# Kernel optimization log

Hardware: AMD Instinct MI355X
Metric: run time of the kernel (lower is better)

## Reference

```python
import jax, jax.numpy as jnp
import numpy as np

N, M, DIST, HEADS, D, C, DFFN = 16384, 16, 2, 8, 256, 64, 512
DH = D // HEADS
GRID = 128
BLOCK = 2048  # mirrors torch batch_size loop in find_neighboring_voxels_optimized
EPS = 1e-5


def _neighbors(coords_f, src, m, dist):
    """Blockwise Manhattan-distance topk neighbor gather.
    coords_f: (N,3) float voxel coords; src: (N,D) features.
    Returns (N, m, D) neighbor features, zero-filled where fewer than m in range."""
    n = coords_f.shape[0]
    qblocks = coords_f.reshape(-1, BLOCK, 3)

    def one_block(cb):
        # (BLOCK, N) Manhattan distances
        d = jnp.abs(cb[:, None, :] - coords_f[None, :, :]).sum(-1)
        d = jnp.where(d <= dist, d, jnp.inf)
        vals, idx = jax.lax.top_k(-d, m)          # nearest m (self first: dist 0)
        valid = (vals > -jnp.inf)[..., None]
        return jnp.where(valid, src[idx], jnp.zeros((), src.dtype))

    return jax.lax.map(one_block, qblocks).reshape(n, m, src.shape[-1])


def _layernorm(x, g, b):
    mu = x.mean(-1, keepdims=True)
    var = ((x - mu) ** 2).mean(-1, keepdims=True)
    return (x - mu) * jax.lax.rsqrt(var + EPS) * g + b


def setup_inputs() -> dict:
    key = jax.random.key(0)
    ks = jax.random.split(key, 32)
    p = lambda i, shape, s: jax.random.normal(ks[i], shape, dtype=jnp.float32) * s
    z = lambda shape: jnp.zeros(shape, dtype=jnp.float32)
    o = lambda shape: jnp.ones(shape, dtype=jnp.float32)
    return {
        "coords": jax.random.randint(ks[0], (N, 3), 0, GRID, dtype=jnp.int32),
        "features": jax.random.normal(ks[1], (N, C), dtype=jnp.float32),
        "pe_w1": p(2, (3, D // 2), 0.5), "pe_b1": z((D // 2,)),
        "pe_w2": p(3, (D // 2, D), 0.08), "pe_b2": z((D,)),
        "proj_w": p(4, (C, D), 0.12), "proj_b": z((D,)),
        "wq": p(5, (D, D), 0.06), "bq": z((D,)),
        "wk": p(6, (D, D), 0.06), "bk": z((D,)),
        "wv": p(7, (D, D), 0.06), "bv": z((D,)),
        "wo": p(8, (D, D), 0.06), "bo": z((D,)),
        "ffn_w1": p(9, (D, DFFN), 0.06), "ffn_b1": z((DFFN,)),
        "ffn_w2": p(10, (DFFN, D), 0.04), "ffn_b2": z((D,)),
        "ln_g": o((D,)), "ln_b": z((D,)),
        "fus_w1": p(11, (D, C), 0.06), "fus_b1": z((C,)),
        "fus_w2": p(12, (2 * C, C), 0.09), "fus_b2": z((C,)),
        "bn_g": o((C,)), "bn_b": z((C,)),
    }


def reference(coords, features, pe_w1, pe_b1, pe_w2, pe_b2, proj_w, proj_b,
              wq, bq, wk, bk, wv, bv, wo, bo,
              ffn_w1, ffn_b1, ffn_w2, ffn_b2, ln_g, ln_b,
              fus_w1, fus_b1, fus_w2, fus_b2, bn_g, bn_b):
    coords_f = coords.astype(jnp.float32)
    # dynamic learnable positional encoding on normalized coords
    xn = coords_f / (GRID - 1)
    pe = jax.nn.relu(xn @ pe_w1 + pe_b1) @ pe_w2 + pe_b2
    src = features @ proj_w + proj_b + pe                       # (N, D)

    nf = _neighbors(coords_f, src, M, DIST)                     # (N, M, D)
    query = nf[:, 0, :]                                         # (N, D) self-feature

    # multihead attention: query len 1, key len M, batch N
    q = (query @ wq + bq).reshape(N, HEADS, DH)
    k = (nf @ wk + bk).reshape(N, M, HEADS, DH)
    v = (nf @ wv + bv).reshape(N, M, HEADS, DH)
    scores = jnp.einsum('nhd,nmhd->nhm', q, k) / jnp.sqrt(jnp.float32(DH))
    attn = jax.nn.softmax(scores, axis=-1)
    ao = jnp.einsum('nhm,nmhd->nhd', attn, v).reshape(N, D) @ wo + bo  # (N, D)

    # FFN with residual + LayerNorm (dropout=0 / eval)
    h = jax.nn.relu(ao @ ffn_w1 + ffn_b1) @ ffn_w2 + ffn_b2
    y = _layernorm(ao + h, ln_g, ln_b)                          # (N, D)

    # EnhancedFusion: project, concat, linear, BatchNorm1d (batch stats), ReLU
    t = y @ fus_w1 + fus_b1                                     # (N, C)
    f = jnp.concatenate([features, t], axis=1) @ fus_w2 + fus_b2
    mu = f.mean(0)
    var = ((f - mu) ** 2).mean(0)
    f = (f - mu) * jax.lax.rsqrt(var + EPS) * bn_g + bn_b
    return jax.nn.relu(f)                                       # (N, C)
```

## Files before the change

### kernel.cpp

```cpp
#include <hip/hip_runtime.h>
#include <stdint.h>

typedef unsigned short u16;
typedef unsigned int   u32;
typedef __attribute__((ext_vector_type(8))) short short8;
typedef __attribute__((ext_vector_type(4))) float f32x4;

static constexpr int kN = 16384;
static constexpr float kEPS = 1e-5f;

__device__ __forceinline__ u16 f2bf(float x) {
  u32 u = __float_as_uint(x);
  u32 r = (u + 0x7fffu + ((u >> 16) & 1u)) >> 16;
  return (u16)r;
}
__device__ __forceinline__ float bf2f(u16 x) {
  return __uint_as_float(((u32)x) << 16);
}
__device__ __forceinline__ void ldbf8(const u16* p, float* o) {
  uint4 v = *(const uint4*)p;
  o[0] = __uint_as_float(v.x << 16);  o[1] = __uint_as_float(v.x & 0xffff0000u);
  o[2] = __uint_as_float(v.y << 16);  o[3] = __uint_as_float(v.y & 0xffff0000u);
  o[4] = __uint_as_float(v.z << 16);  o[5] = __uint_as_float(v.z & 0xffff0000u);
  o[6] = __uint_as_float(v.w << 16);  o[7] = __uint_as_float(v.w & 0xffff0000u);
}
__device__ __forceinline__ void gll16(const u16* g, u16* l) {
  __builtin_amdgcn_global_load_lds(
      (const __attribute__((address_space(1))) void*)g,
      (__attribute__((address_space(3))) void*)l, 16, 0, 0);
}

struct WSet {
  const float* s[8]; u16* d[8];
  int K[8]; int N[8]; int dstride[8]; int coff[8];
};

__global__ __launch_bounds__(256) void k_setup(WSet ws,
                                               u32* __restrict__ zero_area,
                                               const float* __restrict__ proj_b,
                                               const float* __restrict__ pe_b2,
                                               float* __restrict__ pbc,
                                               const float* __restrict__ uw1,
                                               const float* __restrict__ ub1,
                                               const float* __restrict__ uw2,
                                               const float* __restrict__ ub2,
                                               u16* __restrict__ W2f,
                                               float* __restrict__ bbf,
                                               const int* __restrict__ coords,
                                               const float* __restrict__ feats,
                                               const float* __restrict__ pw1,
                                               const float* __restrict__ pb1,
                                               u16* __restrict__ A1,
                                               u16* __restrict__ A2) {
  int w = blockIdx.y;
  if (w == 8) {
    int idx = blockIdx.x * 256 + threadIdx.x;
    if (idx < 33088) zero_area[idx] = 0u;
    return;
  }
  if (w == 9) {
    int bx = blockIdx.x;
    if (bx == 0) {
      pbc[threadIdx.x] = proj_b[threadIdx.x] + pe_b2[threadIdx.x];
    } else if (bx < 65) {
      int n = bx - 1;
      int k = threadIdx.x;
      float s = 0.f;
      for (int j = 0; j < 64; j++) s += uw1[k * 64 + j] * uw2[(64 + j) * 64 + n];
      W2f[n * 320 + k] = f2bf(s);
      if (k < 64) W2f[n * 320 + 256 + k] = f2bf(uw2[k * 64 + n]);
      if (k == 0) {
        float b = ub2[n];
        for (int j = 0; j < 64; j++) b += ub1[j] * uw2[(64 + j) * 64 + n];
        bbf[n] = b;
      }
    }
    return;
  }
  if (w == 10) {
    int r0 = blockIdx.x * 32;
#pragma unroll
    for (int s = 0; s < 3; s++) {
      int j = threadIdx.x + s * 256;
      int row = j / 24, seg = j % 24;
      int n = r0 + row;
      u16 o[8];
      if (seg < 8) {
        const float* fp = feats + (size_t)n * 64 + seg * 8;
        float4 a = *(const float4*)fp;
        float4 b = *(const float4*)(fp + 4);
        o[0] = f2bf(a.x); o[1] = f2bf(a.y); o[2] = f2bf(a.z); o[3] = f2bf(a.w);
        o[4] = f2bf(b.x); o[5] = f2bf(b.y); o[6] = f2bf(b.z); o[7] = f2bf(b.w);
        *(uint4*)(A2 + (size_t)n * 320 + 256 + seg * 8) = *(uint4*)o;
      } else {
        int jj0 = (seg - 8) * 8;
        float x0 = (float)coords[n * 3 + 0] * (1.f / 127.f);
        float x1 = (float)coords[n * 3 + 1] * (1.f / 127.f);
        float x2 = (float)coords[n * 3 + 2] * (1.f / 127.f);
#pragma unroll
        for (int u = 0; u < 8; u++) {
          int jj = jj0 + u;
          float hv = pb1[jj] + x0 * pw1[jj] + x1 * pw1[128 + jj] + x2 * pw1[256 + jj];
          o[u] = f2bf(fmaxf(hv, 0.f));
        }
      }
      *(uint4*)(A1 + (size_t)n * 192 + seg * 8) = *(uint4*)o;
    }
    return;
  }
  const float* S = ws.s[w]; u16* D = ws.d[w];
  int K = ws.K[w], N = ws.N[w], ds = ws.dstride[w], co = ws.coff[w];
  int ntx = N >> 5, tiles = ntx * (K >> 5);
  int t = blockIdx.x;
  if (t >= tiles) return;
  int n0 = (t % ntx) * 32, k0 = (t / ntx) * 32;
  __shared__ float st[32][33];
  int tr = threadIdx.x >> 3, tc4 = (threadIdx.x & 7) * 4;
  float4 v = *(const float4*)(S + (size_t)(k0 + tr) * N + n0 + tc4);
  st[tc4 + 0][tr] = v.x; st[tc4 + 1][tr] = v.y;
  st[tc4 + 2][tr] = v.z; st[tc4 + 3][tr] = v.w;
  __syncthreads();
  u16 o4[4];
  o4[0] = f2bf(st[tr][tc4 + 0]); o4[1] = f2bf(st[tr][tc4 + 1]);
  o4[2] = f2bf(st[tr][tc4 + 2]); o4[3] = f2bf(st[tr][tc4 + 3]);
  *(uint2*)(D + (size_t)(n0 + tr) * ds + co + k0 + tc4) = *(uint2*)o4;
}


__global__ __launch_bounds__(256) void k_hist(const int* __restrict__ coords,
                                              u32* __restrict__ cnt) {
  int n = blockIdx.x * 256 + threadIdx.x;
  int c = coords[n * 3] * 128 + coords[n * 3 + 1];
  atomicAdd(&cnt[c], 1u);
}

__global__ __launch_bounds__(256) void k_scan(const u32* __restrict__ cnt,
                                              u32* __restrict__ startb) {
  __shared__ u32 tots[256];
  int t = threadIdx.x;
  int base = t * 64;
  u32 s = 0;
  for (int i = 0; i < 64; i++) s += cnt[base + i];
  tots[t] = s;
  __syncthreads();
  if (t == 0) {
    u32 run = 0;
    for (int i = 0; i < 256; i++) { u32 v = tots[i]; tots[i] = run; run += v; }
  }
  __syncthreads();
  u32 run = tots[t];
  for (int i = 0; i < 64; i++) { startb[base + i] = run; run += cnt[base + i]; }
}

__global__ __launch_bounds__(256) void k_scatter(const int* __restrict__ coords,
                                                 const u32* __restrict__ startb,
                                                 u32* __restrict__ cursor,
                                                 u32* __restrict__ pts) {
  int n = blockIdx.x * 256 + threadIdx.x;
  int x = coords[n * 3], y = coords[n * 3 + 1], z = coords[n * 3 + 2];
  int c = x * 128 + y;
  u32 slot = atomicAdd(&cursor[c], 1u);
  pts[startb[c] + slot] = ((u32)z << 14) | (u32)n;
}

__global__ __launch_bounds__(256) void k_select(const int* __restrict__ coords,
                                                const u32* __restrict__ startb,
                                                const u32* __restrict__ cnt,
                                                const u32* __restrict__ pts,
                                                int* __restrict__ idxo) {
  int n = blockIdx.x * 256 + threadIdx.x;
  int x = coords[n * 3], y = coords[n * 3 + 1], z = coords[n * 3 + 2];
  u32 best[16];
#pragma unroll
  for (int j = 0; j < 16; j++) best[j] = 0xFFFFFFFFu;
  const int dxs[13] = {0, -1, 1, 0, 0, -2, 2, 0, 0, -1, -1, 1, 1};
  const int dys[13] = {0, 0, 0, -1, 1, 0, 0, -2, 2, -1, 1, -1, 1};
  const int dbs[13] = {0, 1, 1, 1, 1, 2, 2, 2, 2, 2, 2, 2, 2};
#pragma unroll
  for (int t = 0; t < 13; t++) {
    int xx = x + dxs[t], yy = y + dys[t];
    if (xx < 0 || xx > 127 || yy < 0 || yy > 127) continue;
    int c = xx * 128 + yy;
    u32 s0 = startb[c], e0 = s0 + cnt[c];
    for (u32 i = s0; i < e0; ++i) {
      u32 p = pts[i];
      int zq = (int)(p >> 14);
      int id = (int)(p & 16383u);
      int az = z - zq; az = az < 0 ? -az : az;
      int dd = dbs[t] + az;
      u32 key = (dd <= 2) ? (((u32)dd << 14) | (u32)id) : 0xFFFFFFFFu;
#pragma unroll
      for (int j = 0; j < 16; j++) {
        u32 lo = min(best[j], key);
        u32 hi = max(best[j], key);
        best[j] = lo; key = hi;
      }
    }
  }
#pragma unroll
  for (int j = 0; j < 16; j++)
    idxo[n * 16 + j] = (best[j] == 0xFFFFFFFFu) ? -1 : (int)(best[j] & 16383u);
}

template <int ACT, int OUTBF, int ADD>
__global__ __launch_bounds__(256) void k_mfma_gemm(
    const u16* __restrict__ A, const u16* __restrict__ WT,
    const float* __restrict__ bias,
    void* __restrict__ Cout,
    const u16* __restrict__ Addp,
    int M, int K, int N) {
  __shared__ __align__(16) u16 As[2][64 * 32];
  __shared__ __align__(16) u16 Bs[2][64 * 32];
  const int tid = threadIdx.x;
  const int wave = tid >> 6, lane = tid & 63;
  const int bm = blockIdx.y * 64, bn = blockIdx.x * 64;
  const int wr = (wave >> 1) * 32, wc = (wave & 1) * 32;
  const int g = wave * 64 + lane;
  const int grow = g >> 2, gko = (g & 3) * 8;
  const int fr = lane & 15, fk = (lane >> 4) * 8, rq = (lane >> 4) * 4;

  f32x4 acc[2][2];
#pragma unroll
  for (int i = 0; i < 2; i++)
#pragma unroll
    for (int j = 0; j < 2; j++)
#pragma unroll
      for (int r = 0; r < 4; r++) acc[i][j][r] = 0.f;

  for (int k0 = 0; k0 < K; k0 += 64) {
#pragma unroll
    for (int h = 0; h < 2; h++) {
      gll16(A + (size_t)(bm + grow) * K + k0 + h * 32 + gko, As[h] + g * 8);
      gll16(WT + (size_t)(bn + grow) * K + k0 + h * 32 + gko, Bs[h] + g * 8);
    }
    __syncthreads();
#pragma unroll
    for (int h = 0; h < 2; h++) {
      short8 af[2], bg[2];
#pragma unroll
      for (int i = 0; i < 2; i++)
        af[i] = *(const short8*)&As[h][(wr + i * 16 + fr) * 32 + fk];
#pragma unroll
      for (int j = 0; j < 2; j++)
        bg[j] = *(const short8*)&Bs[h][(wc + j * 16 + fr) * 32 + fk];
#pragma unroll
      for (int i = 0; i < 2; i++)
#pragma unroll
        for (int j = 0; j < 2; j++)
          acc[i][j] = __builtin_amdgcn_mfma_f32_16x16x32_bf16(af[i], bg[j], acc[i][j], 0, 0, 0);
    }
    __syncthreads();
  }

#pragma unroll
  for (int j = 0; j < 2; j++) {
    int cc = bn + wc + j * 16 + fr;
    float bval = bias ? bias[cc] : 0.f;
#pragma unroll
    for (int i = 0; i < 2; i++) {
      int rbase = bm + wr + i * 16 + rq;
#pragma unroll
      for (int r = 0; r < 4; r++) {
        float v = acc[i][j][r] + bval;
        size_t o = (size_t)(rbase + r) * N + cc;
        if (ADD) v += bf2f(Addp[o]);
        if (ACT) v = fmaxf(v, 0.f);
        if (OUTBF) ((u16*)Cout)[o] = f2bf(v);
        else       ((float*)Cout)[o] = v;
      }
    }
  }
}

__global__ __launch_bounds__(256) void k_attn(const u16* __restrict__ QKV,
                                              const u32* __restrict__ pts,
                                              const int* __restrict__ idx,
                                              const float* __restrict__ bq,
                                              const float* __restrict__ bk,
                                              const float* __restrict__ bv,
                                              u16* __restrict__ outp) {
  int gid = blockIdx.x * 256 + threadIdx.x;
  int n = (int)(pts[gid >> 3] & 16383u), h = gid & 7;
  const int* ip = idx + n * 16;
  const int hb = h * 32;
  float q[32];
  {
    int i0 = ip[0];
    const u16* qp = QKV + (size_t)i0 * 768 + hb;
#pragma unroll
    for (int j = 0; j < 32; j += 8) ldbf8(qp + j, &q[j]);
#pragma unroll
    for (int j = 0; j < 32; j++) q[j] += bq[hb + j];
  }
  float qbk = 0.f;
#pragma unroll
  for (int j = 0; j < 32; j++) qbk += q[j] * bk[hb + j];
  float s[16]; int ii[16];
#pragma unroll
  for (int m = 0; m < 16; m++) {
    int i = ip[m]; ii[m] = i;
    float d = qbk;
    if (i >= 0) {
      const u16* kp = QKV + (size_t)i * 768 + 256 + hb;
      float kv[32];
#pragma unroll
      for (int j = 0; j < 32; j += 8) ldbf8(kp + j, &kv[j]);
#pragma unroll
      for (int j = 0; j < 32; j++) d += q[j] * kv[j];
    }
    s[m] = d * 0.17677669529663689f;
  }
  float mx = s[0];
#pragma unroll
  for (int m = 1; m < 16; m++) mx = fmaxf(mx, s[m]);
  float sum = 0.f;
#pragma unroll
  for (int m = 0; m < 16; m++) { s[m] = __expf(s[m] - mx); sum += s[m]; }
  float inv = 1.f / sum;
  float o[32];
#pragma unroll
  for (int j = 0; j < 32; j++) o[j] = 0.f;
#pragma unroll
  for (int m = 0; m < 16; m++) {
    if (ii[m] >= 0) {
      const u16* vp = QKV + (size_t)ii[m] * 768 + 512 + hb;
      float vv[32];
#pragma unroll
      for (int j = 0; j < 32; j += 8) ldbf8(vp + j, &vv[j]);
#pragma unroll
      for (int j = 0; j < 32; j++) o[j] += s[m] * vv[j];
    }
  }
  u16* op = outp + (size_t)n * 256 + hb;
#pragma unroll
  for (int j = 0; j < 32; j += 8) {
    u16 tmp[8];
#pragma unroll
    for (int jj = 0; jj < 8; jj++) tmp[jj] = f2bf(o[j + jj] * inv + bv[hb + j + jj]);
    *(uint4*)(op + j) = *(uint4*)tmp;
  }
}

__global__ __launch_bounds__(256) void k_ln(const u16* __restrict__ xx,
                                            const float* __restrict__ g,
                                            const float* __restrict__ b,
                                            u16* __restrict__ A2) {
  int row = blockIdx.x * 4 + (threadIdx.x >> 6);
  int lane = threadIdx.x & 63;
  uint2 raw = *(const uint2*)(xx + (size_t)row * 256 + lane * 4);
  float x0 = __uint_as_float(raw.x << 16), x1 = __uint_as_float(raw.x & 0xffff0000u);
  float x2 = __uint_as_float(raw.y << 16), x3 = __uint_as_float(raw.y & 0xffff0000u);
  float sm = x0 + x1 + x2 + x3;
#pragma unroll
  for (int off = 1; off < 64; off <<= 1) sm += __shfl_xor(sm, off);
  float mu = sm * (1.f / 256.f);
  float d0 = x0 - mu, d1 = x1 - mu, d2 = x2 - mu, d3 = x3 - mu;
  float sq = d0 * d0 + d1 * d1 + d2 * d2 + d3 * d3;
#pragma unroll
  for (int off = 1; off < 64; off <<= 1) sq += __shfl_xor(sq, off);
  float rstd = rsqrtf(sq * (1.f / 256.f) + kEPS);
  float4 gv = *(const float4*)(g + lane * 4);
  float4 bv4 = *(const float4*)(b + lane * 4);
  u16 o[4];
  o[0] = f2bf(d0 * rstd * gv.x + bv4.x); o[1] = f2bf(d1 * rstd * gv.y + bv4.y);
  o[2] = f2bf(d2 * rstd * gv.z + bv4.z); o[3] = f2bf(d3 * rstd * gv.w + bv4.w);
  *(uint2*)(A2 + (size_t)row * 320 + lane * 4) = *(uint2*)o;
}

__global__ __launch_bounds__(256) void k_fgemm(const u16* __restrict__ A2,
                                               const u16* __restrict__ W2f,
                                               const float* __restrict__ bbf,
                                               float* __restrict__ fB,
                                               float* __restrict__ pS,
                                               float* __restrict__ pQ) {
  __shared__ __align__(16) u16 As[2][2048];
  __shared__ __align__(16) u16 Bs[2][2048];
  __shared__ float colS[64][2], colQ[64][2];
  const int tid = threadIdx.x;
  const int wave = tid >> 6, lane = tid & 63;
  const int bm = blockIdx.x * 64;
  const int wr = (wave >> 1) * 32, wc = (wave & 1) * 32;
  const int fr = lane & 15, fk = (lane >> 4) * 8, rq = (lane >> 4) * 4;
  const int g = wave * 64 + lane;
  const int grow = g >> 2, gko = (g & 3) * 8;

  f32x4 acc[2][2];
#pragma unroll
  for (int i = 0; i < 2; i++)
#pragma unroll
    for (int j = 0; j < 2; j++)
#pragma unroll
      for (int r = 0; r < 4; r++) acc[i][j][r] = 0.f;
  for (int k0 = 0; k0 < 320; k0 += 64) {
#pragma unroll
    for (int h = 0; h < 2; h++) {
      gll16(A2 + (size_t)(bm + grow) * 320 + k0 + h * 32 + gko, As[h] + g * 8);
      gll16(W2f + (size_t)grow * 320 + k0 + h * 32 + gko, Bs[h] + g * 8);
    }
    __syncthreads();
#pragma unroll
    for (int h = 0; h < 2; h++) {
      short8 af[2], bg[2];
#pragma unroll
      for (int i = 0; i < 2; i++)
        af[i] = *(const short8*)&As[h][(wr + i * 16 + fr) * 32 + fk];
#pragma unroll
      for (int j = 0; j < 2; j++)
        bg[j] = *(const short8*)&Bs[h][(wc + j * 16 + fr) * 32 + fk];
#pragma unroll
      for (int i = 0; i < 2; i++)
#pragma unroll
        for (int j = 0; j < 2; j++)
          acc[i][j] = __builtin_amdgcn_mfma_f32_16x16x32_bf16(af[i], bg[j], acc[i][j], 0, 0, 0);
    }
    __syncthreads();
  }
  float cS[2] = {0.f, 0.f}, cQ[2] = {0.f, 0.f};
#pragma unroll
  for (int j = 0; j < 2; j++) {
    int col = wc + j * 16 + fr;
    float bv = bbf[col];
#pragma unroll
    for (int i = 0; i < 2; i++) {
      int rbase = bm + wr + i * 16 + rq;
#pragma unroll
      for (int r = 0; r < 4; r++) {
        float v = acc[i][j][r] + bv;
        fB[(size_t)(rbase + r) * 64 + col] = v;
        cS[j] += v; cQ[j] += v * v;
      }
    }
  }
#pragma unroll
  for (int off = 16; off < 64; off <<= 1) {
#pragma unroll
    for (int j = 0; j < 2; j++) {
      cS[j] += __shfl_xor(cS[j], off);
      cQ[j] += __shfl_xor(cQ[j], off);
    }
  }
  if ((lane >> 4) == 0) {
#pragma unroll
    for (int j = 0; j < 2; j++) {
      colS[wc + j * 16 + fr][wave >> 1] = cS[j];
      colQ[wc + j * 16 + fr][wave >> 1] = cQ[j];
    }
  }
  __syncthreads();
  if (tid < 64) {
    atomicAdd(&pS[tid], colS[tid][0] + colS[tid][1]);
    atomicAdd(&pQ[tid], colQ[tid][0] + colQ[tid][1]);
  }
}

__global__ __launch_bounds__(64) void k_bnfin(const float* __restrict__ pS,
                                              const float* __restrict__ pQ,
                                              const float* __restrict__ g,
                                              const float* __restrict__ b,
                                              float* __restrict__ coef,
                                              float* __restrict__ shift) {
  int c = threadIdx.x;
  float S = pS[c], Q = pQ[c];
  float m = S * (1.f / 16384.f);
  float var = Q * (1.f / 16384.f) - m * m;
  float cf = rsqrtf(var + kEPS) * g[c];
  coef[c] = cf;
  shift[c] = b[c] - m * cf;
}

__global__ __launch_bounds__(256) void k_bnapply(const float* __restrict__ f,
                                                 const float* __restrict__ coef,
                                                 const float* __restrict__ shift,
                                                 float* __restrict__ out) {
  int gid = blockIdx.x * 256 + threadIdx.x;
  int e = gid * 4, col = e & 63;
  float4 v = *(const float4*)(f + e);
  float4 cf = *(const float4*)(coef + col);
  float4 sh = *(const float4*)(shift + col);
  float4 o;
  o.x = fmaxf(v.x * cf.x + sh.x, 0.f);
  o.y = fmaxf(v.y * cf.y + sh.y, 0.f);
  o.z = fmaxf(v.z * cf.z + sh.z, 0.f);
  o.w = fmaxf(v.w * cf.w + sh.w, 0.f);
  *(float4*)(out + e) = o;
}

extern "C" void kernel_launch(void* const* d_in, const int* in_sizes, int n_in,
                              void* d_out, int out_size, void* d_ws, size_t ws_size,
                              hipStream_t stream) {
  (void)in_sizes; (void)n_in; (void)out_size; (void)ws_size;
  const int*   coords = (const int*)d_in[0];
  const float* feats  = (const float*)d_in[1];
  const float* pe_w1  = (const float*)d_in[2];
  const float* pe_b1  = (const float*)d_in[3];
  const float* pe_w2  = (const float*)d_in[4];
  const float* pe_b2  = (const float*)d_in[5];
  const float* proj_w = (const float*)d_in[6];
  const float* proj_b = (const float*)d_in[7];
  const float* wq  = (const float*)d_in[8];
  const float* bq  = (const float*)d_in[9];
  const float* wk  = (const float*)d_in[10];
  const float* bk  = (const float*)d_in[11];
  const float* wv  = (const float*)d_in[12];
  const float* bv  = (const float*)d_in[13];
  const float* wo  = (const float*)d_in[14];
  const float* bo  = (const float*)d_in[15];
  const float* fw1 = (const float*)d_in[16];
  const float* fb1 = (const float*)d_in[17];
  const float* fw2 = (const float*)d_in[18];
  const float* fb2 = (const float*)d_in[19];
  const float* lng = (const float*)d_in[20];
  const float* lnb = (const float*)d_in[21];
  const float* uw1 = (const float*)d_in[22];
  const float* ub1 = (const float*)d_in[23];
  const float* uw2 = (const float*)d_in[24];
  const float* ub2 = (const float*)d_in[25];
  const float* bng = (const float*)d_in[26];
  const float* bnb = (const float*)d_in[27];
  float* out = (float*)d_out;

  char* Wc = (char*)d_ws;
  const size_t MB = 1u << 20;
  u16*   A1    = (u16*)(Wc + 0 * MB);
  u16*   srcb  = (u16*)(Wc + 6 * MB);
  u16*   QKVb  = (u16*)(Wc + 14 * MB);
  u16*   aoInB = (u16*)(Wc + 38 * MB);
  u16*   aoB   = (u16*)(Wc + 46 * MB);
  u16*   h1B   = (u16*)(Wc + 54 * MB);
  u16*   xBb   = (u16*)(Wc + 70 * MB);
  u16*   A2    = (u16*)(Wc + 78 * MB);
  float* fB    = (float*)(Wc + 0 * MB);

  u16* qkvT  = (u16*)(Wc + 88 * MB);
  u16* woT   = qkvT + 196608;
  u16* fw1T  = woT + 65536;
  u16* fw2T  = fw1T + 131072;
  u16* W1T   = fw2T + 131072;
  u16* W2f   = W1T + 49152;
  float* pbc = (float*)(W2f + 20480);
  float* bbf = pbc + 256;

  u32* Z      = (u32*)(Wc + 90 * MB);
  u32* cnt    = Z;
  u32* cursor = Z + 16384;
  float* pS   = (float*)(Z + 32768);
  float* pQ   = (float*)(Z + 32832);
  float* coefb = (float*)(Z + 32912);
  float* shb   = coefb + 64;
  u32* startb = Z + 33280;
  u32* pts    = Z + 49664;
  int* idxb   = (int*)(Z + 66048);

  WSet ws;
  ws.s[0] = wq;     ws.d[0] = qkvT;          ws.K[0] = 256; ws.N[0] = 256; ws.dstride[0] = 256; ws.coff[0] = 0;
  ws.s[1] = wk;     ws.d[1] = qkvT + 65536;  ws.K[1] = 256; ws.N[1] = 256; ws.dstride[1] = 256; ws.coff[1] = 0;
  ws.s[2] = wv;     ws.d[2] = qkvT + 131072; ws.K[2] = 256; ws.N[2] = 256; ws.dstride[2] = 256; ws.coff[2] = 0;
  ws.s[3] = wo;     ws.d[3] = woT;           ws.K[3] = 256; ws.N[3] = 256; ws.dstride[3] = 256; ws.coff[3] = 0;
  ws.s[4] = fw1;    ws.d[4] = fw1T;          ws.K[4] = 256; ws.N[4] = 512; ws.dstride[4] = 256; ws.coff[4] = 0;
  ws.s[5] = fw2;    ws.d[5] = fw2T;          ws.K[5] = 512; ws.N[5] = 256; ws.dstride[5] = 512; ws.coff[5] = 0;
  ws.s[6] = proj_w; ws.d[6] = W1T;           ws.K[6] = 64;  ws.N[6] = 256; ws.dstride[6] = 192; ws.coff[6] = 0;
  ws.s[7] = pe_w2;  ws.d[7] = W1T;           ws.K[7] = 128; ws.N[7] = 256; ws.dstride[7] = 192; ws.coff[7] = 64;

  k_setup<<<dim3(512, 11), 256, 0, stream>>>(ws, Z, proj_b, pe_b2, pbc,
                                             uw1, ub1, uw2, ub2, W2f, bbf,
                                             coords, feats, pe_w1, pe_b1, A1, A2);
  k_hist<<<64, 256, 0, stream>>>(coords, cnt);
  k_scan<<<1, 256, 0, stream>>>(cnt, startb);
  k_scatter<<<64, 256, 0, stream>>>(coords, startb, cursor, pts);
  k_select<<<64, 256, 0, stream>>>(coords, startb, cnt, pts, idxb);
  k_mfma_gemm<0, 1, 0><<<dim3(4, 256), 256, 0, stream>>>(A1, W1T, pbc, srcb, nullptr, kN, 192, 256);
  k_mfma_gemm<0, 1, 0><<<dim3(12, 256), 256, 0, stream>>>(srcb, qkvT, nullptr, QKVb, nullptr, kN, 256, 768);
  k_attn<<<512, 256, 0, stream>>>(QKVb, pts, idxb, bq, bk, bv, aoInB);
  k_mfma_gemm<0, 1, 0><<<dim3(4, 256), 256, 0, stream>>>(aoInB, woT, bo, aoB, nullptr, kN, 256, 256);
  k_mfma_gemm<1, 1, 0><<<dim3(8, 256), 256, 0, stream>>>(aoB, fw1T, fb1, h1B, nullptr, kN, 256, 512);
  k_mfma_gemm<0, 1, 1><<<dim3(4, 256), 256, 0, stream>>>(h1B, fw2T, fb2, xBb, aoB, kN, 512, 256);
  k_ln<<<4096, 256, 0, stream>>>(xBb, lng, lnb, A2);
  k_fgemm<<<256, 256, 0, stream>>>(A2, W2f, bbf, fB, pS, pQ);
  k_bnfin<<<1, 64, 0, stream>>>(pS, pQ, bng, bnb, coefb, shb);
  k_bnapply<<<1024, 256, 0, stream>>>(fB, coefb, shb, out);
}
```

Measured before the change: 248.1 us.

## Fold input projection into QKV weights and enlarge MFMA GEMM tiles

```diff
diff --git a/kernel.cpp b/kernel.cpp
--- a/kernel.cpp
+++ b/kernel.cpp
@@ -31,15 +31,14 @@
 }
 
 struct WSet {
-  const float* s[8]; u16* d[8];
-  int K[8]; int N[8]; int dstride[8]; int coff[8];
+  const float* s[6]; u16* d[6];
+  int K[6]; int N[6]; int dstride[6]; int coff[6];
 };
 
 __global__ __launch_bounds__(256) void k_setup(WSet ws,
                                                u32* __restrict__ zero_area,
                                                const float* __restrict__ proj_b,
                                                const float* __restrict__ pe_b2,
-                                               float* __restrict__ pbc,
                                                const float* __restrict__ uw1,
                                                const float* __restrict__ ub1,
                                                const float* __restrict__ uw2,
@@ -51,33 +50,36 @@
                                                const float* __restrict__ pw1,
                                                const float* __restrict__ pb1,
                                                u16* __restrict__ A1,
-                                               u16* __restrict__ A2) {
+                                               u16* __restrict__ A2,
+                                               const float* __restrict__ wq,
+                                               const float* __restrict__ wk,
+                                               const float* __restrict__ wv,
+                                               const float* __restrict__ proj_w_f,
+                                               const float* __restrict__ pe_w2_f,
+                                               u16* __restrict__ W1K,
+                                               float* __restrict__ bcomb) {
   int w = blockIdx.y;
-  if (w == 8) {
+  if (w == 6) {
     int idx = blockIdx.x * 256 + threadIdx.x;
     if (idx < 33088) zero_area[idx] = 0u;
     return;
   }
-  if (w == 9) {
-    int bx = blockIdx.x;
-    if (bx == 0) {
-      pbc[threadIdx.x] = proj_b[threadIdx.x] + pe_b2[threadIdx.x];
-    } else if (bx < 65) {
-      int n = bx - 1;
-      int k = threadIdx.x;
-      float s = 0.f;
-      for (int j = 0; j < 64; j++) s += uw1[k * 64 + j] * uw2[(64 + j) * 64 + n];
-      W2f[n * 320 + k] = f2bf(s);
-      if (k < 64) W2f[n * 320 + 256 + k] = f2bf(uw2[k * 64 + n]);
-      if (k == 0) {
-        float b = ub2[n];
-        for (int j = 0; j < 64; j++) b += ub1[j] * uw2[(64 + j) * 64 + n];
-        bbf[n] = b;
-      }
+  if (w == 7) {
+    int n = blockIdx.x;
+    if (n >= 64) return;
+    int k = threadIdx.x;
+    float s = 0.f;
+    for (int j = 0; j < 64; j++) s += uw1[k * 64 + j] * uw2[(64 + j) * 64 + n];
+    W2f[n * 320 + k] = f2bf(s);
+    if (k < 64) W2f[n * 320 + 256 + k] = f2bf(uw2[k * 64 + n]);
+    if (k == 0) {
+      float b = ub2[n];
+      for (int j = 0; j < 64; j++) b += ub1[j] * uw2[(64 + j) * 64 + n];
+      bbf[n] = b;
     }
     return;
   }
-  if (w == 10) {
+  if (w == 8) {
     int r0 = blockIdx.x * 32;
 #pragma unroll
     for (int s = 0; s < 3; s++) {
@@ -108,6 +110,26 @@
     }
     return;
   }
+  if (w == 9) {
+    int bx = blockIdx.x;
+    if (bx < 3) {
+      const float* wsel = (bx == 0) ? wq : (bx == 1) ? wk : wv;
+      int c = threadIdx.x;
+      float s = 0.f;
+      for (int d = 0; d < 256; d++) s += (proj_b[d] + pe_b2[d]) * wsel[d * 256 + c];
+      bcomb[bx * 256 + c] = s;
+    } else if (bx < 27) {
+      int i0 = (bx - 3) * 2048 + threadIdx.x * 8;
+      const float* src = (i0 < 16384) ? (proj_w_f + i0) : (pe_w2_f + (i0 - 16384));
+      float4 a = *(const float4*)src;
+      float4 b = *(const float4*)(src + 4);
+      u16 o[8];
+      o[0] = f2bf(a.x); o[1] = f2bf(a.y); o[2] = f2bf(a.z); o[3] = f2bf(a.w);
+      o[4] = f2bf(b.x); o[5] = f2bf(b.y); o[6] = f2bf(b.z); o[7] = f2bf(b.w);
+      *(uint4*)(W1K + i0) = *(uint4*)o;
+    }
+    return;
+  }
   const float* S = ws.s[w]; u16* D = ws.d[w];
   int K = ws.K[w], N = ws.N[w], ds = ws.dstride[w], co = ws.coff[w];
   int ntx = N >> 5, tiles = ntx * (K >> 5);
@@ -202,62 +224,72 @@
     idxo[n * 16 + j] = (best[j] == 0xFFFFFFFFu) ? -1 : (int)(best[j] & 16383u);
 }
 
-template <int ACT, int OUTBF, int ADD>
-__global__ __launch_bounds__(256) void k_mfma_gemm(
+template <int BM, int BN, int ACT, int OUTBF, int ADD>
+__global__ __launch_bounds__(256) void k_mgemm(
     const u16* __restrict__ A, const u16* __restrict__ WT,
     const float* __restrict__ bias,
     void* __restrict__ Cout,
     const u16* __restrict__ Addp,
     int M, int K, int N) {
-  __shared__ __align__(16) u16 As[2][64 * 32];
-  __shared__ __align__(16) u16 Bs[2][64 * 32];
+  constexpr int FM = BM / 32, FN = BN / 32;
+  constexpr int RA = BM / 64, RB = BN / 64;
+  __shared__ __align__(16) u16 As[2][BM * 32];
+  __shared__ __align__(16) u16 Bs[2][BN * 32];
   const int tid = threadIdx.x;
   const int wave = tid >> 6, lane = tid & 63;
-  const int bm = blockIdx.y * 64, bn = blockIdx.x * 64;
-  const int wr = (wave >> 1) * 32, wc = (wave & 1) * 32;
-  const int g = wave * 64 + lane;
-  const int grow = g >> 2, gko = (g & 3) * 8;
+  const int bm = blockIdx.y * BM, bn = blockIdx.x * BN;
+  const int wr = (wave >> 1) * (BM / 2), wc = (wave & 1) * (BN / 2);
   const int fr = lane & 15, fk = (lane >> 4) * 8, rq = (lane >> 4) * 4;
 
-  f32x4 acc[2][2];
-#pragma unroll
-  for (int i = 0; i < 2; i++)
-#pragma unroll
-    for (int j = 0; j < 2; j++)
+  f32x4 acc[FM][FN];
+#pragma unroll
+  for (int i = 0; i < FM; i++)
+#pragma unroll
+    for (int j = 0; j < FN; j++)
 #pragma unroll
       for (int r = 0; r < 4; r++) acc[i][j][r] = 0.f;
 
   for (int k0 = 0; k0 < K; k0 += 64) {
 #pragma unroll
     for (int h = 0; h < 2; h++) {
-      gll16(A + (size_t)(bm + grow) * K + k0 + h * 32 + gko, As[h] + g * 8);
-      gll16(WT + (size_t)(bn + grow) * K + k0 + h * 32 + gko, Bs[h] + g * 8);
+#pragma unroll
+      for (int r = 0; r < RA; r++) {
+        int g2 = r * 256 + tid;
+        gll16(A + (size_t)(bm + (g2 >> 2)) * K + k0 + h * 32 + (g2 & 3) * 8,
+              As[h] + g2 * 8);
+      }
+#pragma unroll
+      for (int r = 0; r < RB; r++) {
+        int g2 = r * 256 + tid;
+        gll16(WT + (size_t)(bn + (g2 >> 2)) * K + k0 + h * 32 + (g2 & 3) * 8,
+              Bs[h] + g2 * 8);
+      }
     }
     __syncthreads();
 #pragma unroll
     for (int h = 0; h < 2; h++) {
-      short8 af[2], bg[2];
-#pragma unroll
-      for (int i = 0; i < 2; i++)
+      short8 af[FM], bg[FN];
+#pragma unroll
+      for (int i = 0; i < FM; i++)
         af[i] = *(const short8*)&As[h][(wr + i * 16 + fr) * 32 + fk];
 #pragma unroll
-      for (int j = 0; j < 2; j++)
+      for (int j = 0; j < FN; j++)
         bg[j] = *(const short8*)&Bs[h][(wc + j * 16 + fr) * 32 + fk];
 #pragma unroll
-      for (int i = 0; i < 2; i++)
-#pragma unroll
-        for (int j = 0; j < 2; j++)
+      for (int i = 0; i < FM; i++)
+#pragma unroll
+        for (int j = 0; j < FN; j++)
           acc[i][j] = __builtin_amdgcn_mfma_f32_16x16x32_bf16(af[i], bg[j], acc[i][j], 0, 0, 0);
     }
     __syncthreads();
   }
 
 #pragma unroll
-  for (int j = 0; j < 2; j++) {
+  for (int j = 0; j < FN; j++) {
     int cc = bn + wc + j * 16 + fr;
     float bval = bias ? bias[cc] : 0.f;
 #pragma unroll
-    for (int i = 0; i < 2; i++) {
+    for (int i = 0; i < FM; i++) {
       int rbase = bm + wr + i * 16 + rq;
 #pragma unroll
       for (int r = 0; r < 4; r++) {
@@ -522,7 +554,6 @@
   char* Wc = (char*)d_ws;
   const size_t MB = 1u << 20;
   u16*   A1    = (u16*)(Wc + 0 * MB);
-  u16*   srcb  = (u16*)(Wc + 6 * MB);
   u16*   QKVb  = (u16*)(Wc + 14 * MB);
   u16*   aoInB = (u16*)(Wc + 38 * MB);
   u16*   aoB   = (u16*)(Wc + 46 * MB);
@@ -535,10 +566,11 @@
   u16* woT   = qkvT + 196608;
   u16* fw1T  = woT + 65536;
   u16* fw2T  = fw1T + 131072;
-  u16* W1T   = fw2T + 131072;
-  u16* W2f   = W1T + 49152;
-  float* pbc = (float*)(W2f + 20480);
-  float* bbf = pbc + 256;
+  u16* W1K   = fw2T + 131072;
+  u16* W2f   = W1K + 49152;
+  u16* Wcomb = W2f + 20480;
+  float* bbf   = (float*)(Wcomb + 147456);
+  float* bcomb = bbf + 64;
 
   u32* Z      = (u32*)(Wc + 90 * MB);
   u32* cnt    = Z;
@@ -558,22 +590,26 @@
   ws.s[3] = wo;     ws.d[3] = woT;           ws.K[3] = 256; ws.N[3] = 256; ws.dstride[3] = 256; ws.coff[3] = 0;
   ws.s[4] = fw1;    ws.d[4] = fw1T;          ws.K[4] = 256; ws.N[4] = 512; ws.dstride[4] = 256; ws.coff[4] = 0;
   ws.s[5] = fw2;    ws.d[5] = fw2T;          ws.K[5] = 512; ws.N[5] = 256; ws.dstride[5] = 512; ws.coff[5] = 0;
-  ws.s[6] = proj_w; ws.d[6] = W1T;           ws.K[6] = 64;  ws.N[6] = 256; ws.dstride[6] = 192; ws.coff[6] = 0;
-  ws.s[7] = pe_w2;  ws.d[7] = W1T;           ws.K[7] = 128; ws.N[7] = 256; ws.dstride[7] = 192; ws.coff[7] = 64;
-
-  k_setup<<<dim3(512, 11), 256, 0, stream>>>(ws, Z, proj_b, pe_b2, pbc,
+
+  k_setup<<<dim3(512, 10), 256, 0, stream>>>(ws, Z, proj_b, pe_b2,
                                              uw1, ub1, uw2, ub2, W2f, bbf,
-                                             coords, feats, pe_w1, pe_b1, A1, A2);
+                                             coords, feats, pe_w1, pe_b1, A1, A2,
+                                             wq, wk, wv, proj_w, pe_w2, W1K, bcomb);
+  k_mgemm<64, 64, 0, 1, 0><<<dim3(3, 12), 256, 0, stream>>>(
+      qkvT, W1K, nullptr, Wcomb, nullptr, 768, 256, 192);
   k_hist<<<64, 256, 0, stream>>>(coords, cnt);
   k_scan<<<1, 256, 0, stream>>>(cnt, startb);
   k_scatter<<<64, 256, 0, stream>>>(coords, startb, cursor, pts);
   k_select<<<64, 256, 0, stream>>>(coords, startb, cnt, pts, idxb);
-  k_mfma_gemm<0, 1, 0><<<dim3(4, 256), 256, 0, stream>>>(A1, W1T, pbc, srcb, nullptr, kN, 192, 256);
-  k_mfma_gemm<0, 1, 0><<<dim3(12, 256), 256, 0, stream>>>(srcb, qkvT, nullptr, QKVb, nullptr, kN, 256, 768);
+  k_mgemm<128, 128, 0, 1, 0><<<dim3(6, 128), 256, 0, stream>>>(
+      A1, Wcomb, bcomb, QKVb, nullptr, kN, 192, 768);
   k_attn<<<512, 256, 0, stream>>>(QKVb, pts, idxb, bq, bk, bv, aoInB);
-  k_mfma_gemm<0, 1, 0><<<dim3(4, 256), 256, 0, stream>>>(aoInB, woT, bo, aoB, nullptr, kN, 256, 256);
-  k_mfma_gemm<1, 1, 0><<<dim3(8, 256), 256, 0, stream>>>(aoB, fw1T, fb1, h1B, nullptr, kN, 256, 512);
-  k_mfma_gemm<0, 1, 1><<<dim3(4, 256), 256, 0, stream>>>(h1B, fw2T, fb2, xBb, aoB, kN, 512, 256);
+  k_mgemm<128, 64, 0, 1, 0><<<dim3(4, 128), 256, 0, stream>>>(
+      aoInB, woT, bo, aoB, nullptr, kN, 256, 256);
+  k_mgemm<128, 128, 1, 1, 0><<<dim3(4, 128), 256, 0, stream>>>(
+      aoB, fw1T, fb1, h1B, nullptr, kN, 256, 512);
+  k_mgemm<128, 64, 0, 1, 1><<<dim3(4, 128), 256, 0, stream>>>(
+      h1B, fw2T, fb2, xBb, aoB, kN, 512, 256);
   k_ln<<<4096, 256, 0, stream>>>(xBb, lng, lnb, A2);
   k_fgemm<<<256, 256, 0, stream>>>(A2, W2f, bbf, fB, pS, pQ);
   k_bnfin<<<1, 64, 0, stream>>>(pS, pQ, bng, bnb, coefb, shb);
```

After: 249.4 us. No clear change (+0.5%).
